# Kernel tuning notes

Hardware: AMD Instinct MI355X
Metric: run time of the kernel (lower is better)

The kernel has to match this reference:

```python
import jax, jax.numpy as jnp
import numpy as np

N = 50000      # n_nodes
E = 300000     # n_edges
R = 32         # n_relations
D = 256        # embedding_dim
H = 128        # bilstm_hidden_size (2H == D so gate dims line up, as the source requires)
I = 64         # input_dim (time-series feature dim)
B = 4096       # batch
S = 50         # seq_len
HOPS = 2       # context_hops


def setup_inputs() -> dict:
    key = jax.random.key(0)
    ks = jax.random.split(key, 20)
    sc = 0.02
    inp = {
        "ts": jax.random.normal(ks[0], (B, S, I), jnp.float32),
        "node_emb": jax.random.normal(ks[1], (N, D), jnp.float32) * sc,
        "rel_w": jax.random.normal(ks[2], (R, D), jnp.float32) * sc + 1.0,
        "gate_W": jax.random.normal(ks[3], (D, 2 * D), jnp.float32) * sc,
        "gate_b": jnp.zeros((D,), jnp.float32),
        "risk_W1": jax.random.normal(ks[4], (D, D), jnp.float32) * sc,
        "risk_b1": jnp.zeros((D,), jnp.float32),
        "risk_W2": jax.random.normal(ks[5], (D, D), jnp.float32) * sc,
        "risk_b2": jnp.zeros((D,), jnp.float32),
        # BiLSTM encoder params (torch gate order i,f,g,o), fwd + bwd directions
        "Wih_f": jax.random.normal(ks[6], (4 * H, I), jnp.float32) * sc,
        "Whh_f": jax.random.normal(ks[7], (4 * H, H), jnp.float32) * sc,
        "b_f": jnp.zeros((4 * H,), jnp.float32),
        "Wih_b": jax.random.normal(ks[8], (4 * H, I), jnp.float32) * sc,
        "Whh_b": jax.random.normal(ks[9], (4 * H, H), jnp.float32) * sc,
        "b_b": jnp.zeros((4 * H,), jnp.float32),
        "edge_index": jax.random.randint(ks[10], (2, E), 0, N, jnp.int32),
        "edge_type": jax.random.randint(ks[11], (E,), 0, R, jnp.int32),
        "node_indexes": jax.random.randint(ks[12], (B,), 0, N, jnp.int32),
    }
    return inp


def _lstm_dir(x, Wih, Whh, b, reverse):
    # x: [B, S, I] -> outputs [B, S, H]
    def step(carry, xt):
        h, c = carry
        g = xt @ Wih.T + h @ Whh.T + b          # [B, 4H]
        i, f, gg, o = jnp.split(g, 4, axis=-1)
        c = jax.nn.sigmoid(f) * c + jax.nn.sigmoid(i) * jnp.tanh(gg)
        h = jax.nn.sigmoid(o) * jnp.tanh(c)
        return (h, c), h
    h0 = jnp.zeros((x.shape[0], Whh.shape[1]), x.dtype)
    xs = jnp.swapaxes(x, 0, 1)                   # [S, B, I]
    _, hs = jax.lax.scan(step, (h0, h0), xs, reverse=reverse)
    return jnp.swapaxes(hs, 0, 1)                # [B, S, H]


def _gcn(emb, head, tail, edge_type, rel_w, n_hops):
    # relation-weighted multi-hop message passing: gather -> relation scale -> scatter-mean
    deg = jax.ops.segment_sum(jnp.ones((head.shape[0],), emb.dtype), head, num_segments=N)
    deg = jnp.clip(deg, 1.0)[:, None]
    out = emb
    acc = emb
    for _ in range(n_hops):
        msg = out[tail] * rel_w[edge_type]                      # [E, D]
        out = jax.ops.segment_sum(msg, head, num_segments=N) / deg
        acc = acc + out
    return acc / (n_hops + 1.0)


def reference(ts, node_emb, rel_w, gate_W, gate_b, risk_W1, risk_b1, risk_W2,
              risk_b2, Wih_f, Whh_f, b_f, Wih_b, Whh_b, b_b,
              edge_index, edge_type, node_indexes):
    head, tail = edge_index[0], edge_index[1]
    all_emb = _gcn(node_emb, head, tail, edge_type, rel_w, HOPS)
    struct = all_emb[node_indexes]                              # [B, D]
    # BiLSTM encoder, temporal embedding = mean over time of [B,S,2H]
    hf = _lstm_dir(ts, Wih_f, Whh_f, b_f, reverse=False)
    hb = _lstm_dir(ts, Wih_b, Whh_b, b_b, reverse=True)
    temporal = jnp.concatenate([hf, hb], axis=-1).mean(axis=1)  # [B, 2H] == [B, D]
    cat = jnp.concatenate([struct, temporal], axis=-1)          # [B, 2D]
    gate = jax.nn.sigmoid(cat @ gate_W.T + gate_b)              # [B, D]
    merged = gate * struct + (1.0 - gate) * temporal
    risk = jnp.tanh(merged @ risk_W1.T + risk_b1) @ risk_W2.T + risk_b2
    return jax.nn.sigmoid(risk.sum(axis=-1))                    # [B]
```

## Files before the change

### kernel.cpp

```cpp
#include <hip/hip_runtime.h>

#define N_NODES 50000
#define N_EDGES 300000
#define DIM 256
#define HID 128
#define INP 64
#define BATCH 4096
#define SEQ 50
#define SCAN_BLOCKS 196

typedef float f32x2 __attribute__((ext_vector_type(2)));
typedef float f32x4 __attribute__((ext_vector_type(4)));
typedef __bf16 bf16x2 __attribute__((ext_vector_type(2)));
typedef __bf16 bf16x4 __attribute__((ext_vector_type(4)));
typedef __bf16 bf16x8 __attribute__((ext_vector_type(8)));

#define L2E  1.4426950408889634f
#define L2E2 2.8853900817779268f

__device__ __forceinline__ float sigmoidf_(float x) {
    return __builtin_amdgcn_rcpf(1.0f + __expf(-x));
}
__device__ __forceinline__ float tanhf_(float x) {
    return 1.0f - 2.0f * __builtin_amdgcn_rcpf(1.0f + __expf(2.0f * x));
}
__device__ __forceinline__ float sigp_(float y) {
    return __builtin_amdgcn_rcpf(1.0f + __builtin_amdgcn_exp2f(-y));
}
__device__ __forceinline__ float tanhp_(float y) {
    return 1.0f - 2.0f * __builtin_amdgcn_rcpf(1.0f + __builtin_amdgcn_exp2f(y));
}
__device__ __forceinline__ float tanhc_(float x) {
    return 1.0f - 2.0f * __builtin_amdgcn_rcpf(1.0f + __builtin_amdgcn_exp2f(x * L2E2));
}

__device__ __forceinline__ void barrier_lds_only() {
    asm volatile("s_waitcnt lgkmcnt(0)" ::: "memory");
    __builtin_amdgcn_s_barrier();
}

__global__ void k_prep(const float* __restrict__ Wih_f, const float* __restrict__ Whh_f,
                       const float* __restrict__ Wih_b, const float* __restrict__ Whh_b,
                       const float* __restrict__ gate_W, const float* __restrict__ risk_W1,
                       const float* __restrict__ risk_W2, const float* __restrict__ risk_b2,
                       const float* __restrict__ node_emb,
                       __bf16* __restrict__ w2frag, __bf16* __restrict__ gwp,
                       __bf16* __restrict__ w1p, float* __restrict__ w2s,
                       int* __restrict__ deg, int* __restrict__ flagi,
                       __bf16* __restrict__ embh) {
    __shared__ float red[256];
    int bid = blockIdx.x, tid = threadIdx.x;
    if (bid < 768) {
        int idx = bid * 256 + tid;
        int dir = idx / 98304;
        int rem = idx % 98304;
        int frag = rem >> 9;
        int within = rem & 511;
        int lane = within >> 3, j = within & 7;
        int kc = frag % 6;
        int wg = frag / 6;
        int g = wg & 3, w = wg >> 2;
        int n = g * 128 + w * 16 + (lane & 15);
        int k = kc * 32 + (lane >> 4) * 8 + j;
        const float* Wih = dir ? Wih_b : Wih_f;
        const float* Whh = dir ? Whh_b : Whh_f;
        float v = (k < 64) ? Wih[n * 64 + k] : Whh[n * 128 + (k - 64)];
        float sc = (g == 2) ? L2E2 : L2E;
        w2frag[idx] = (__bf16)(v * sc);
    } else if (bid < 1280) {
        int idx = (bid - 768) * 256 + tid;
        int frag = idx >> 9, within = idx & 511;
        int lane = within >> 3, j = within & 7;
        int kc = frag % 16, T = frag / 16;
        int n = T * 16 + (lane & 15);
        int k = kc * 32 + (lane >> 4) * 8 + j;
        gwp[idx] = (__bf16)gate_W[(size_t)n * 512 + k];
    } else if (bid < 1536) {
        int idx = (bid - 1280) * 256 + tid;
        int frag = idx >> 9, within = idx & 511;
        int lane = within >> 3, j = within & 7;
        int kc = frag % 8, T = frag / 8;
        int n = T * 16 + (lane & 15);
        int k = kc * 32 + (lane >> 4) * 8 + j;
        w1p[idx] = (__bf16)risk_W1[(size_t)n * 256 + k];
    } else if (bid == 1536) {
        int k = tid;
        float s = 0.0f;
        for (int n = 0; n < 256; n++) s += risk_W2[(size_t)n * 256 + k];
        w2s[k] = s;
        red[k] = risk_b2[k];
        __syncthreads();
        for (int st = 128; st > 0; st >>= 1) {
            if (k < st) red[k] += red[k + st];
            __syncthreads();
        }
        if (k == 0) w2s[256] = red[0];
    } else if (bid < 1733) {
        int i = (bid - 1537) * 256 + tid;
        if (i < N_NODES) deg[i] = 0;
    } else if (bid < 1782) {
        int i = (bid - 1733) * 256 + tid;
        flagi[i] = 0;
    } else {
        int idx = (bid - 1782) * 2048 + tid * 8;
        f32x4 a = *(const f32x4*)(node_emb + idx);
        f32x4 b = *(const f32x4*)(node_emb + idx + 4);
        bf16x8 o;
        o[0] = (__bf16)a.x; o[1] = (__bf16)a.y; o[2] = (__bf16)a.z; o[3] = (__bf16)a.w;
        o[4] = (__bf16)b.x; o[5] = (__bf16)b.y; o[6] = (__bf16)b.z; o[7] = (__bf16)b.w;
        *(bf16x8*)(embh + idx) = o;
    }
}


__global__ void k_hist(const int* __restrict__ head, int* __restrict__ deg) {
    int e = blockIdx.x * 256 + threadIdx.x;
    if (e < N_EDGES) atomicAdd(&deg[head[e]], 1);
}

__global__ void k_bsum(const int* __restrict__ deg, int* __restrict__ bsum) {
    __shared__ int red[256];
    int n = blockIdx.x * 256 + threadIdx.x;
    red[threadIdx.x] = (n < N_NODES) ? deg[n] : 0;
    __syncthreads();
    for (int st = 128; st > 0; st >>= 1) {
        if (threadIdx.x < st) red[threadIdx.x] += red[threadIdx.x + st];
        __syncthreads();
    }
    if (threadIdx.x == 0) bsum[blockIdx.x] = red[0];
}

__global__ void k_scanb(const int* __restrict__ bsum, int* __restrict__ boff) {
    __shared__ int s[256];
    int i = threadIdx.x;
    int v = (i < SCAN_BLOCKS) ? bsum[i] : 0;
    s[i] = v;
    __syncthreads();
    for (int st = 1; st < 256; st <<= 1) {
        int add = (i >= st) ? s[i - st] : 0;
        __syncthreads();
        s[i] += add;
        __syncthreads();
    }
    boff[i] = s[i] - v;
}

__global__ void k_scan2(const int* __restrict__ deg, const int* __restrict__ boff,
                        int* __restrict__ offsets, int* __restrict__ cursor) {
    __shared__ int s[256];
    int i = threadIdx.x;
    int n = blockIdx.x * 256 + i;
    int v = (n < N_NODES) ? deg[n] : 0;
    s[i] = v;
    __syncthreads();
    for (int st = 1; st < 256; st <<= 1) {
        int add = (i >= st) ? s[i - st] : 0;
        __syncthreads();
        s[i] += add;
        __syncthreads();
    }
    if (n < N_NODES) {
        int off = boff[blockIdx.x] + s[i] - v;
        offsets[n] = off;
        cursor[n] = off;
    }
    if (n == 0) offsets[N_NODES] = N_EDGES;
}

__global__ void k_place(const int* __restrict__ head, const int* __restrict__ tail,
                        const int* __restrict__ etype, int* __restrict__ cursor,
                        int* __restrict__ sorted) {
    int e = blockIdx.x * 256 + threadIdx.x;
    if (e >= N_EDGES) return;
    int h = head[e];
    int pos = atomicAdd(&cursor[h], 1);
    sorted[pos] = tail[e] | (etype[e] << 16);
}

__global__ void k_flag(const int* __restrict__ nidx, const int* __restrict__ offsets,
                       const int* __restrict__ sorted, char* __restrict__ flag) {
    int tid = threadIdx.x;
    int w = tid >> 6, lane = tid & 63;
    int b = blockIdx.x * 4 + w;
    int n = nidx[b];
    if (lane == 0) flag[n] = 1;
    int s = offsets[n], e = offsets[n + 1];
    for (int j = s + lane; j < e; j += 64) flag[sorted[j] & 0xFFFF] = 1;
}

__global__ void k_gather(const int* __restrict__ offsets, const int* __restrict__ sorted,
                         const float* __restrict__ relw, const __bf16* __restrict__ srch,
                         const char* __restrict__ flag, __bf16* __restrict__ dst) {
    int tid = threadIdx.x;
    int w = tid >> 6, lane = tid & 63;
    int n = blockIdx.x * 4 + w;
    if (n >= N_NODES) return;
    if (!flag[n]) return;
    int s = offsets[n], e = offsets[n + 1];
    f32x4 acc0 = (f32x4){0.f, 0.f, 0.f, 0.f};
    f32x4 acc1 = (f32x4){0.f, 0.f, 0.f, 0.f};
    f32x4 acc2 = (f32x4){0.f, 0.f, 0.f, 0.f};
    f32x4 acc3 = (f32x4){0.f, 0.f, 0.f, 0.f};
    int j = s;
    for (; j + 4 <= e; j += 4) {
        int p0 = sorted[j], p1 = sorted[j + 1], p2 = sorted[j + 2], p3 = sorted[j + 3];
        bf16x4 v0 = *(const bf16x4*)(srch + (size_t)(p0 & 0xFFFF) * DIM + lane * 4);
        bf16x4 v1 = *(const bf16x4*)(srch + (size_t)(p1 & 0xFFFF) * DIM + lane * 4);
        bf16x4 v2 = *(const bf16x4*)(srch + (size_t)(p2 & 0xFFFF) * DIM + lane * 4);
        bf16x4 v3 = *(const bf16x4*)(srch + (size_t)(p3 & 0xFFFF) * DIM + lane * 4);
        f32x4 f0 = (f32x4){(float)v0[0], (float)v0[1], (float)v0[2], (float)v0[3]};
        f32x4 f1 = (f32x4){(float)v1[0], (float)v1[1], (float)v1[2], (float)v1[3]};
        f32x4 f2 = (f32x4){(float)v2[0], (float)v2[1], (float)v2[2], (float)v2[3]};
        f32x4 f3 = (f32x4){(float)v3[0], (float)v3[1], (float)v3[2], (float)v3[3]};
        acc0 += f0 * *(const f32x4*)(relw + (p0 >> 16) * DIM + lane * 4);
        acc1 += f1 * *(const f32x4*)(relw + (p1 >> 16) * DIM + lane * 4);
        acc2 += f2 * *(const f32x4*)(relw + (p2 >> 16) * DIM + lane * 4);
        acc3 += f3 * *(const f32x4*)(relw + (p3 >> 16) * DIM + lane * 4);
    }
    for (; j < e; j++) {
        int p0 = sorted[j];
        bf16x4 v0 = *(const bf16x4*)(srch + (size_t)(p0 & 0xFFFF) * DIM + lane * 4);
        f32x4 f0 = (f32x4){(float)v0[0], (float)v0[1], (float)v0[2], (float)v0[3]};
        acc0 += f0 * *(const f32x4*)(relw + (p0 >> 16) * DIM + lane * 4);
    }
    acc0 = (acc0 + acc1) + (acc2 + acc3);
    float inv = 1.0f / fmaxf((float)(e - s), 1.0f);
    acc0 *= inv;
    bf16x4 o;
    o[0] = (__bf16)acc0.x; o[1] = (__bf16)acc0.y; o[2] = (__bf16)acc0.z; o[3] = (__bf16)acc0.w;
    *(bf16x4*)(dst + (size_t)n * DIM + lane * 4) = o;
}

__global__ void k_gather2(const int* __restrict__ nidx, const int* __restrict__ offsets,
                          const int* __restrict__ sorted, const float* __restrict__ relw,
                          const __bf16* __restrict__ out1h, const __bf16* __restrict__ embh,
                          float* __restrict__ structb) {
    int tid = threadIdx.x;
    int w = tid >> 6, lane = tid & 63;
    int b = blockIdx.x * 4 + w;
    int n = nidx[b];
    int s = offsets[n], e = offsets[n + 1];
    f32x4 acc0 = (f32x4){0.f, 0.f, 0.f, 0.f};
    f32x4 acc1 = (f32x4){0.f, 0.f, 0.f, 0.f};
    f32x4 acc2 = (f32x4){0.f, 0.f, 0.f, 0.f};
    f32x4 acc3 = (f32x4){0.f, 0.f, 0.f, 0.f};
    int j = s;
    for (; j + 4 <= e; j += 4) {
        int p0 = sorted[j], p1 = sorted[j + 1], p2 = sorted[j + 2], p3 = sorted[j + 3];
        bf16x4 v0 = *(const bf16x4*)(out1h + (size_t)(p0 & 0xFFFF) * DIM + lane * 4);
        bf16x4 v1 = *(const bf16x4*)(out1h + (size_t)(p1 & 0xFFFF) * DIM + lane * 4);
        bf16x4 v2 = *(const bf16x4*)(out1h + (size_t)(p2 & 0xFFFF) * DIM + lane * 4);
        bf16x4 v3 = *(const bf16x4*)(out1h + (size_t)(p3 & 0xFFFF) * DIM + lane * 4);
        f32x4 f0 = (f32x4){(float)v0[0], (float)v0[1], (float)v0[2], (float)v0[3]};
        f32x4 f1 = (f32x4){(float)v1[0], (float)v1[1], (float)v1[2], (float)v1[3]};
        f32x4 f2 = (f32x4){(float)v2[0], (float)v2[1], (float)v2[2], (float)v2[3]};
        f32x4 f3 = (f32x4){(float)v3[0], (float)v3[1], (float)v3[2], (float)v3[3]};
        acc0 += f0 * *(const f32x4*)(relw + (p0 >> 16) * DIM + lane * 4);
        acc1 += f1 * *(const f32x4*)(relw + (p1 >> 16) * DIM + lane * 4);
        acc2 += f2 * *(const f32x4*)(relw + (p2 >> 16) * DIM + lane * 4);
        acc3 += f3 * *(const f32x4*)(relw + (p3 >> 16) * DIM + lane * 4);
    }
    for (; j < e; j++) {
        int p0 = sorted[j];
        bf16x4 v0 = *(const bf16x4*)(out1h + (size_t)(p0 & 0xFFFF) * DIM + lane * 4);
        f32x4 f0 = (f32x4){(float)v0[0], (float)v0[1], (float)v0[2], (float)v0[3]};
        acc0 += f0 * *(const f32x4*)(relw + (p0 >> 16) * DIM + lane * 4);
    }
    acc0 = (acc0 + acc1) + (acc2 + acc3);
    float inv = 1.0f / fmaxf((float)(e - s), 1.0f);
    f32x4 o2 = acc0 * inv;
    bf16x4 eh = *(const bf16x4*)(embh + (size_t)n * DIM + lane * 4);
    bf16x4 o1h = *(const bf16x4*)(out1h + (size_t)n * DIM + lane * 4);
    f32x4 e0 = (f32x4){(float)eh[0], (float)eh[1], (float)eh[2], (float)eh[3]};
    f32x4 o1 = (f32x4){(float)o1h[0], (float)o1h[1], (float)o1h[2], (float)o1h[3]};
    *(f32x4*)(structb + (size_t)b * DIM + lane * 4) = (e0 + o1 + o2) * (1.0f / 3.0f);
}

__launch_bounds__(512)
__global__ void k_lstm(const float* __restrict__ ts, const __bf16* __restrict__ w2frag,
                       const float* __restrict__ b_f, const float* __restrict__ b_b,
                       float* __restrict__ temporal) {
    int dir = blockIdx.y;
    int btile = blockIdx.x;
    int tid = threadIdx.x;
    int w = tid >> 6;
    int lane = tid & 63;
    int col = lane & 15, quad = lane >> 4;

    __shared__ __align__(16) __bf16 SA[2 * 16 * 200];
    __shared__ __align__(16) __bf16 SB[2 * 16 * 200];

    for (int i = tid; i < 2048; i += 512) {
        int m = i >> 7, k = i & 127;
        SA[m * 200 + 64 + k] = (__bf16)0.0f;
        SB[m * 200 + 64 + k] = (__bf16)0.0f;
    }

    const float* bias = dir ? b_b : b_f;
    f32x4 bva[4];
#pragma unroll
    for (int g = 0; g < 4; g++) {
        float b = bias[g * 128 + w * 16 + col] * ((g == 2) ? L2E2 : L2E);
        bva[g] = (f32x4){b, b, b, b};
    }

    const __bf16* wbase = w2frag + (size_t)dir * 98304 + (size_t)w * 12288;
    bf16x8 wreg[24];
#pragma unroll
    for (int f = 0; f < 24; f++) {
        wreg[f] = *(const bf16x8*)(wbase + (f << 9) + lane * 8);
    }

    int sm = tid >> 5, sc = (tid & 31) * 2;
    const float* xbA = ts + ((size_t)(btile * 32 + sm) * SEQ) * INP + sc;
    const float* xbB = ts + ((size_t)(btile * 32 + 16 + sm) * SEQ) * INP + sc;
    int t0i = dir ? (SEQ - 1) : 0;
    int t1i = dir ? (SEQ - 2) : 1;
    {
        f32x2 xa = *(const f32x2*)(xbA + (size_t)t0i * INP);
        f32x2 xb = *(const f32x2*)(xbB + (size_t)t0i * INP);
        bf16x2 va; va[0] = (__bf16)xa.x; va[1] = (__bf16)xa.y;
        bf16x2 vb; vb[0] = (__bf16)xb.x; vb[1] = (__bf16)xb.y;
        *(bf16x2*)&SA[sm * 200 + sc] = va;
        *(bf16x2*)&SB[sm * 200 + sc] = vb;
    }
    f32x2 xpreA = *(const f32x2*)(xbA + (size_t)t1i * INP);
    f32x2 xpreB = *(const f32x2*)(xbB + (size_t)t1i * INP);
    int xdelta = dir ? -INP : INP;
    const float* pA = xbA + (size_t)(dir ? (SEQ - 3) : 2) * INP;
    const float* pB = xbB + (size_t)(dir ? (SEQ - 3) : 2) * INP;

    f32x4 cA = (f32x4){0.f, 0.f, 0.f, 0.f}, hsA = cA;
    f32x4 cB = cA, hsB = cA;
    f32x4 accA[4], accB[4];
    int hwr = quad * 4 * 200 + 64 + w * 16 + col;
    int ard = col * 200 + quad * 8;
    barrier_lds_only();

    {
        bf16x8 a0 = *(const bf16x8*)&SA[ard];
#pragma unroll
        for (int g = 0; g < 4; g++)
            accA[g] = __builtin_amdgcn_mfma_f32_16x16x32_bf16(a0, wreg[g * 6], bva[g], 0, 0, 0);
    }
#pragma unroll
    for (int kc = 1; kc < 6; kc++) {
        bf16x8 a0 = *(const bf16x8*)&SA[ard + kc * 32];
#pragma unroll
        for (int g = 0; g < 4; g++)
            accA[g] = __builtin_amdgcn_mfma_f32_16x16x32_bf16(a0, wreg[g * 6 + kc], accA[g], 0, 0, 0);
    }

    for (int t = 0; t < SEQ; t++) {
        int cb = (t & 1) * 3200;
        int nb = ((t + 1) & 1) * 3200;

        f32x2 xnA;
        bool ld = (t + 2 < SEQ);
        if (ld) { xnA = *(const f32x2*)pA; pA += xdelta; }
        {
            bf16x8 a0 = *(const bf16x8*)&SB[cb + ard];
#pragma unroll
            for (int g = 0; g < 4; g++)
                accB[g] = __builtin_amdgcn_mfma_f32_16x16x32_bf16(a0, wreg[g * 6], bva[g], 0, 0, 0);
        }
#pragma unroll
        for (int kc = 1; kc < 6; kc++) {
            bf16x8 a0 = *(const bf16x8*)&SB[cb + ard + kc * 32];
#pragma unroll
            for (int g = 0; g < 4; g++)
                accB[g] = __builtin_amdgcn_mfma_f32_16x16x32_bf16(a0, wreg[g * 6 + kc], accB[g], 0, 0, 0);
        }
#pragma unroll
        for (int r = 0; r < 4; r++) {
            float c = sigp_(accA[1][r]) * cA[r] + sigp_(accA[0][r]) * tanhp_(accA[2][r]);
            float h = sigp_(accA[3][r]) * tanhc_(c);
            cA[r] = c;
            hsA[r] += h;
            SA[nb + hwr + r * 200] = (__bf16)h;
        }
        if (t + 1 < SEQ) {
            bf16x2 v; v[0] = (__bf16)xpreA.x; v[1] = (__bf16)xpreA.y;
            *(bf16x2*)&SA[nb + sm * 200 + sc] = v;
            if (ld) xpreA = xnA;
        }
        barrier_lds_only();

        f32x2 xnB;
        if (ld) { xnB = *(const f32x2*)pB; pB += xdelta; }
        if (t + 1 < SEQ) {
            {
                bf16x8 a0 = *(const bf16x8*)&SA[nb + ard];
#pragma unroll
                for (int g = 0; g < 4; g++)
                    accA[g] = __builtin_amdgcn_mfma_f32_16x16x32_bf16(a0, wreg[g * 6], bva[g], 0, 0, 0);
            }
#pragma unroll
            for (int kc = 1; kc < 6; kc++) {
                bf16x8 a0 = *(const bf16x8*)&SA[nb + ard + kc * 32];
#pragma unroll
                for (int g = 0; g < 4; g++)
                    accA[g] = __builtin_amdgcn_mfma_f32_16x16x32_bf16(a0, wreg[g * 6 + kc], accA[g], 0, 0, 0);
            }
        }
#pragma unroll
        for (int r = 0; r < 4; r++) {
            float c = sigp_(accB[1][r]) * cB[r] + sigp_(accB[0][r]) * tanhp_(accB[2][r]);
            float h = sigp_(accB[3][r]) * tanhc_(c);
            cB[r] = c;
            hsB[r] += h;
            SB[nb + hwr + r * 200] = (__bf16)h;
        }
        if (t + 1 < SEQ) {
            bf16x2 v; v[0] = (__bf16)xpreB.x; v[1] = (__bf16)xpreB.y;
            *(bf16x2*)&SB[nb + sm * 200 + sc] = v;
            if (ld) xpreB = xnB;
        }
        barrier_lds_only();
    }

#pragma unroll
    for (int r = 0; r < 4; r++) {
        int j = w * 16 + col;
        int bA = btile * 32 + quad * 4 + r;
        int bB = bA + 16;
        temporal[(size_t)bA * 256 + dir * 128 + j] = hsA[r] * (1.0f / SEQ);
        temporal[(size_t)bB * 256 + dir * 128 + j] = hsB[r] * (1.0f / SEQ);
    }
}


__launch_bounds__(256)
__global__ void k_head(const float* __restrict__ structb, const float* __restrict__ temporal,
                       const __bf16* __restrict__ gwp, const __bf16* __restrict__ w1p,
                       const float* __restrict__ gate_b, const float* __restrict__ risk_b1,
                       const float* __restrict__ w2s, float* __restrict__ out) {
    int bt = blockIdx.x;
    int tid = threadIdx.x;
    int w = tid >> 6, lane = tid & 63;
    int col = lane & 15, quad = lane >> 4;

    __shared__ __align__(16) __bf16 cat[16][520];
    __shared__ __align__(16) __bf16 mbuf[16][264];
    __shared__ float sacc[16];

    for (int i = tid; i < 16 * 512; i += 256) {
        int m = i >> 9, k = i & 511;
        int b = bt * 16 + m;
        float v = (k < 256) ? structb[(size_t)b * 256 + k]
                            : temporal[(size_t)b * 256 + (k - 256)];
        cat[m][k] = (__bf16)v;
    }
    if (tid < 16) sacc[tid] = 0.0f;
    __syncthreads();

    f32x4 acc[4];
#pragma unroll
    for (int ct = 0; ct < 4; ct++) {
        float b = gate_b[w * 64 + ct * 16 + col];
        acc[ct] = (f32x4){b, b, b, b};
    }
#pragma unroll
    for (int kc = 0; kc < 16; kc++) {
        bf16x8 a = *(const bf16x8*)&cat[col][kc * 32 + quad * 8];
#pragma unroll
        for (int ct = 0; ct < 4; ct++) {
            bf16x8 bf = *(const bf16x8*)(gwp + (((w * 4 + ct) * 16 + kc) << 9) + lane * 8);
            acc[ct] = __builtin_amdgcn_mfma_f32_16x16x32_bf16(a, bf, acc[ct], 0, 0, 0);
        }
    }
#pragma unroll
    for (int ct = 0; ct < 4; ct++) {
        int n = w * 64 + ct * 16 + col;
#pragma unroll
        for (int r = 0; r < 4; r++) {
            int m = quad * 4 + r;
            int b = bt * 16 + m;
            float g = sigmoidf_(acc[ct][r]);
            float s = structb[(size_t)b * 256 + n];
            float tm = temporal[(size_t)b * 256 + n];
            mbuf[m][n] = (__bf16)(g * s + (1.0f - g) * tm);
        }
    }
    __syncthreads();

    f32x4 acc2[4];
#pragma unroll
    for (int ct = 0; ct < 4; ct++) {
        float b = risk_b1[w * 64 + ct * 16 + col];
        acc2[ct] = (f32x4){b, b, b, b};
    }
#pragma unroll
    for (int kc = 0; kc < 8; kc++) {
        bf16x8 a = *(const bf16x8*)&mbuf[col][kc * 32 + quad * 8];
#pragma unroll
        for (int ct = 0; ct < 4; ct++) {
            bf16x8 bf = *(const bf16x8*)(w1p + (((w * 4 + ct) * 8 + kc) << 9) + lane * 8);
            acc2[ct] = __builtin_amdgcn_mfma_f32_16x16x32_bf16(a, bf, acc2[ct], 0, 0, 0);
        }
    }
    float part[4] = {0.f, 0.f, 0.f, 0.f};
#pragma unroll
    for (int ct = 0; ct < 4; ct++) {
        int n = w * 64 + ct * 16 + col;
        float wv = w2s[n];
#pragma unroll
        for (int r = 0; r < 4; r++) {
            part[r] += tanhf_(acc2[ct][r]) * wv;
        }
    }
#pragma unroll
    for (int off = 1; off < 16; off <<= 1) {
#pragma unroll
        for (int r = 0; r < 4; r++) part[r] += __shfl_xor(part[r], off, 64);
    }
    if (col == 0) {
#pragma unroll
        for (int r = 0; r < 4; r++) atomicAdd(&sacc[quad * 4 + r], part[r]);
    }
    __syncthreads();
    if (tid < 16) out[bt * 16 + tid] = sigmoidf_(sacc[tid] + w2s[256]);
}


extern "C" void kernel_launch(void* const* d_in, const int* in_sizes, int n_in,
                              void* d_out, int out_size, void* d_ws, size_t ws_size,
                              hipStream_t stream) {
    const float* ts       = (const float*)d_in[0];
    const float* node_emb = (const float*)d_in[1];
    const float* rel_w    = (const float*)d_in[2];
    const float* gate_W   = (const float*)d_in[3];
    const float* gate_b   = (const float*)d_in[4];
    const float* risk_W1  = (const float*)d_in[5];
    const float* risk_b1  = (const float*)d_in[6];
    const float* risk_W2  = (const float*)d_in[7];
    const float* risk_b2  = (const float*)d_in[8];
    const float* Wih_f    = (const float*)d_in[9];
    const float* Whh_f    = (const float*)d_in[10];
    const float* b_f      = (const float*)d_in[11];
    const float* Wih_b    = (const float*)d_in[12];
    const float* Whh_b    = (const float*)d_in[13];
    const float* b_b      = (const float*)d_in[14];
    const int* edge_index = (const int*)d_in[15];
    const int* edge_type  = (const int*)d_in[16];
    const int* node_idx   = (const int*)d_in[17];
    const int* head = edge_index;
    const int* tail = edge_index + N_EDGES;
    float* out = (float*)d_out;

    char* ws = (char*)d_ws;
    const size_t o_deg      = 0;
    const size_t o_flagbuf  = 200704;
    const size_t o_bsum     = o_flagbuf + 50176;
    const size_t o_boff     = o_bsum + 1024;
    const size_t o_offsets  = o_boff + 1024;
    const size_t o_cursor   = o_offsets + 200960;
    const size_t o_sorted   = o_cursor + 200704;
    const size_t o_out1     = o_sorted + 1200128;
    const size_t o_embh     = o_out1 + 25600000;
    const size_t o_temporal = o_embh + 25600000;
    const size_t o_struct   = o_temporal + 4194304;
    const size_t o_gwp      = o_struct + 4194304;
    const size_t o_w1p      = o_gwp + 262144;
    const size_t o_w2s      = o_w1p + 131072;
    const size_t o_w2frag   = o_w2s + 2048;

    int*    deg      = (int*)(ws + o_deg);
    char*   flag     = (char*)(ws + o_flagbuf);
    int*    flagi    = (int*)(ws + o_flagbuf);
    int*    bsum     = (int*)(ws + o_bsum);
    int*    boff     = (int*)(ws + o_boff);
    int*    offsets  = (int*)(ws + o_offsets);
    int*    cursor   = (int*)(ws + o_cursor);
    int*    sorted   = (int*)(ws + o_sorted);
    __bf16* out1h    = (__bf16*)(ws + o_out1);
    __bf16* embh     = (__bf16*)(ws + o_embh);
    float*  temporal = (float*)(ws + o_temporal);
    float*  structb  = (float*)(ws + o_struct);
    __bf16* gwp      = (__bf16*)(ws + o_gwp);
    __bf16* w1p      = (__bf16*)(ws + o_w1p);
    float*  w2s      = (float*)(ws + o_w2s);
    __bf16* w2frag   = (__bf16*)(ws + o_w2frag);

    k_prep<<<8032, 256, 0, stream>>>(Wih_f, Whh_f, Wih_b, Whh_b, gate_W, risk_W1,
                                     risk_W2, risk_b2, node_emb, w2frag, gwp, w1p,
                                     w2s, deg, flagi, embh);
    k_hist<<<(N_EDGES + 255) / 256, 256, 0, stream>>>(head, deg);
    k_bsum<<<SCAN_BLOCKS, 256, 0, stream>>>(deg, bsum);
    k_scanb<<<1, 256, 0, stream>>>(bsum, boff);
    k_scan2<<<SCAN_BLOCKS, 256, 0, stream>>>(deg, boff, offsets, cursor);
    k_place<<<(N_EDGES + 255) / 256, 256, 0, stream>>>(head, tail, edge_type, cursor, sorted);
    k_flag<<<BATCH / 4, 256, 0, stream>>>(node_idx, offsets, sorted, flag);
    k_gather<<<(N_NODES + 3) / 4, 256, 0, stream>>>(offsets, sorted, rel_w, embh, flag, out1h);
    k_lstm<<<dim3(BATCH / 32, 2), 512, 0, stream>>>(ts, w2frag, b_f, b_b, temporal);
    k_gather2<<<BATCH / 4, 256, 0, stream>>>(node_idx, offsets, sorted, rel_w, out1h, embh, structb);
    k_head<<<BATCH / 16, 256, 0, stream>>>(structb, temporal, gwp, w1p, gate_b, risk_b1, w2s, out);
}
```

Measured before the change: 317.0 us.

## Split LSTM kernel into one 16-row tile per block, doubling grid

The LSTM kernel no longer interleaves two 16-row batch tiles (A/B ping-pong) within a block. Each block now handles a single 16-row tile, and the grid doubles from 128x2 to 256x2 blocks. This exposes more blocks to fill the GPU's compute units and halves LDS use per block. In exchange it gives up the intra-block overlap in which one tile's MFMA work hid the other tile's activation math and barrier latency, and every block must reload the recurrent weights into registers.

```diff
diff --git a/kernel.cpp b/kernel.cpp
--- a/kernel.cpp
+++ b/kernel.cpp
@@ -231,6 +231,104 @@
     *(bf16x4*)(dst + (size_t)n * DIM + lane * 4) = o;
 }
 
+__launch_bounds__(512)
+__global__ void k_lstm(const float* __restrict__ ts, const __bf16* __restrict__ w2frag,
+                       const float* __restrict__ b_f, const float* __restrict__ b_b,
+                       float* __restrict__ temporal) {
+    int dir = blockIdx.y;
+    int btile = blockIdx.x;
+    int tid = threadIdx.x;
+    int w = tid >> 6;
+    int lane = tid & 63;
+    int col = lane & 15, quad = lane >> 4;
+
+    __shared__ __align__(16) __bf16 S[2 * 16 * 200];
+
+    for (int i = tid; i < 2048; i += 512) {
+        int m = i >> 7, k = i & 127;
+        S[m * 200 + 64 + k] = (__bf16)0.0f;
+    }
+
+    const float* bias = dir ? b_b : b_f;
+    f32x4 bva[4];
+#pragma unroll
+    for (int g = 0; g < 4; g++) {
+        float b = bias[g * 128 + w * 16 + col] * ((g == 2) ? L2E2 : L2E);
+        bva[g] = (f32x4){b, b, b, b};
+    }
+
+    const __bf16* wbase = w2frag + (size_t)dir * 98304 + (size_t)w * 12288;
+    bf16x8 wreg[24];
+#pragma unroll
+    for (int f = 0; f < 24; f++) {
+        wreg[f] = *(const bf16x8*)(wbase + (f << 9) + lane * 8);
+    }
+
+    int sm = tid >> 5, sc = (tid & 31) * 2;
+    const float* xb = ts + ((size_t)(btile * 16 + sm) * SEQ) * INP + sc;
+    int t0i = dir ? (SEQ - 1) : 0;
+    int t1i = dir ? (SEQ - 2) : 1;
+    {
+        f32x2 xa = *(const f32x2*)(xb + (size_t)t0i * INP);
+        bf16x2 va; va[0] = (__bf16)xa.x; va[1] = (__bf16)xa.y;
+        *(bf16x2*)&S[sm * 200 + sc] = va;
+    }
+    f32x2 xpre = *(const f32x2*)(xb + (size_t)t1i * INP);
+    int xdelta = dir ? -INP : INP;
+    const float* p = xb + (size_t)(dir ? (SEQ - 3) : 2) * INP;
+
+    f32x4 c = (f32x4){0.f, 0.f, 0.f, 0.f}, hs = c;
+    f32x4 acc[4];
+    int hwr = quad * 4 * 200 + 64 + w * 16 + col;
+    int ard = col * 200 + quad * 8;
+    barrier_lds_only();
+
+    for (int t = 0; t < SEQ; t++) {
+        int cb = (t & 1) * 3200;
+        int nb = ((t + 1) & 1) * 3200;
+
+        f32x2 xn;
+        bool ld = (t + 2 < SEQ);
+        if (ld) { xn = *(const f32x2*)p; p += xdelta; }
+
+        {
+            bf16x8 a0 = *(const bf16x8*)&S[cb + ard];
+#pragma unroll
+            for (int g = 0; g < 4; g++)
+                acc[g] = __builtin_amdgcn_mfma_f32_16x16x32_bf16(a0, wreg[g * 6], bva[g], 0, 0, 0);
+        }
+#pragma unroll
+        for (int kc = 1; kc < 6; kc++) {
+            bf16x8 a0 = *(const bf16x8*)&S[cb + ard + kc * 32];
+#pragma unroll
+            for (int g = 0; g < 4; g++)
+                acc[g] = __builtin_amdgcn_mfma_f32_16x16x32_bf16(a0, wreg[g * 6 + kc], acc[g], 0, 0, 0);
+        }
+
+#pragma unroll
+        for (int r = 0; r < 4; r++) {
+            float cc = sigp_(acc[1][r]) * c[r] + sigp_(acc[0][r]) * tanhp_(acc[2][r]);
+            float h = sigp_(acc[3][r]) * tanhc_(cc);
+            c[r] = cc;
+            hs[r] += h;
+            S[nb + hwr + r * 200] = (__bf16)h;
+        }
+        if (t + 1 < SEQ) {
+            bf16x2 v; v[0] = (__bf16)xpre.x; v[1] = (__bf16)xpre.y;
+            *(bf16x2*)&S[nb + sm * 200 + sc] = v;
+            if (ld) xpre = xn;
+        }
+        barrier_lds_only();
+    }
+
+#pragma unroll
+    for (int r = 0; r < 4; r++) {
+        int j = w * 16 + col;
+        int b = btile * 16 + quad * 4 + r;
+        temporal[(size_t)b * 256 + dir * 128 + j] = hs[r] * (1.0f / SEQ);
+    }
+}
+
 __global__ void k_gather2(const int* __restrict__ nidx, const int* __restrict__ offsets,
                           const int* __restrict__ sorted, const float* __restrict__ relw,
                           const __bf16* __restrict__ out1h, const __bf16* __restrict__ embh,
@@ -276,159 +374,6 @@
     *(f32x4*)(structb + (size_t)b * DIM + lane * 4) = (e0 + o1 + o2) * (1.0f / 3.0f);
 }
 
-__launch_bounds__(512)
-__global__ void k_lstm(const float* __restrict__ ts, const __bf16* __restrict__ w2frag,
-                       const float* __restrict__ b_f, const float* __restrict__ b_b,
-                       float* __restrict__ temporal) {
-    int dir = blockIdx.y;
-    int btile = blockIdx.x;
-    int tid = threadIdx.x;
-    int w = tid >> 6;
-    int lane = tid & 63;
-    int col = lane & 15, quad = lane >> 4;
-
-    __shared__ __align__(16) __bf16 SA[2 * 16 * 200];
-    __shared__ __align__(16) __bf16 SB[2 * 16 * 200];
-
-    for (int i = tid; i < 2048; i += 512) {
-        int m = i >> 7, k = i & 127;
-        SA[m * 200 + 64 + k] = (__bf16)0.0f;
-        SB[m * 200 + 64 + k] = (__bf16)0.0f;
-    }
-
-    const float* bias = dir ? b_b : b_f;
-    f32x4 bva[4];
-#pragma unroll
-    for (int g = 0; g < 4; g++) {
-        float b = bias[g * 128 + w * 16 + col] * ((g == 2) ? L2E2 : L2E);
-        bva[g] = (f32x4){b, b, b, b};
-    }
-
-    const __bf16* wbase = w2frag + (size_t)dir * 98304 + (size_t)w * 12288;
-    bf16x8 wreg[24];
-#pragma unroll
-    for (int f = 0; f < 24; f++) {
-        wreg[f] = *(const bf16x8*)(wbase + (f << 9) + lane * 8);
-    }
-
-    int sm = tid >> 5, sc = (tid & 31) * 2;
-    const float* xbA = ts + ((size_t)(btile * 32 + sm) * SEQ) * INP + sc;
-    const float* xbB = ts + ((size_t)(btile * 32 + 16 + sm) * SEQ) * INP + sc;
-    int t0i = dir ? (SEQ - 1) : 0;
-    int t1i = dir ? (SEQ - 2) : 1;
-    {
-        f32x2 xa = *(const f32x2*)(xbA + (size_t)t0i * INP);
-        f32x2 xb = *(const f32x2*)(xbB + (size_t)t0i * INP);
-        bf16x2 va; va[0] = (__bf16)xa.x; va[1] = (__bf16)xa.y;
-        bf16x2 vb; vb[0] = (__bf16)xb.x; vb[1] = (__bf16)xb.y;
-        *(bf16x2*)&SA[sm * 200 + sc] = va;
-        *(bf16x2*)&SB[sm * 200 + sc] = vb;
-    }
-    f32x2 xpreA = *(const f32x2*)(xbA + (size_t)t1i * INP);
-    f32x2 xpreB = *(const f32x2*)(xbB + (size_t)t1i * INP);
-    int xdelta = dir ? -INP : INP;
-    const float* pA = xbA + (size_t)(dir ? (SEQ - 3) : 2) * INP;
-    const float* pB = xbB + (size_t)(dir ? (SEQ - 3) : 2) * INP;
-
-    f32x4 cA = (f32x4){0.f, 0.f, 0.f, 0.f}, hsA = cA;
-    f32x4 cB = cA, hsB = cA;
-    f32x4 accA[4], accB[4];
-    int hwr = quad * 4 * 200 + 64 + w * 16 + col;
-    int ard = col * 200 + quad * 8;
-    barrier_lds_only();
-
-    {
-        bf16x8 a0 = *(const bf16x8*)&SA[ard];
-#pragma unroll
-        for (int g = 0; g < 4; g++)
-            accA[g] = __builtin_amdgcn_mfma_f32_16x16x32_bf16(a0, wreg[g * 6], bva[g], 0, 0, 0);
-    }
-#pragma unroll
-    for (int kc = 1; kc < 6; kc++) {
-        bf16x8 a0 = *(const bf16x8*)&SA[ard + kc * 32];
-#pragma unroll
-        for (int g = 0; g < 4; g++)
-            accA[g] = __builtin_amdgcn_mfma_f32_16x16x32_bf16(a0, wreg[g * 6 + kc], accA[g], 0, 0, 0);
-    }
-
-    for (int t = 0; t < SEQ; t++) {
-        int cb = (t & 1) * 3200;
-        int nb = ((t + 1) & 1) * 3200;
-
-        f32x2 xnA;
-        bool ld = (t + 2 < SEQ);
-        if (ld) { xnA = *(const f32x2*)pA; pA += xdelta; }
-        {
-            bf16x8 a0 = *(const bf16x8*)&SB[cb + ard];
-#pragma unroll
-            for (int g = 0; g < 4; g++)
-                accB[g] = __builtin_amdgcn_mfma_f32_16x16x32_bf16(a0, wreg[g * 6], bva[g], 0, 0, 0);
-        }
-#pragma unroll
-        for (int kc = 1; kc < 6; kc++) {
-            bf16x8 a0 = *(const bf16x8*)&SB[cb + ard + kc * 32];
-#pragma unroll
-            for (int g = 0; g < 4; g++)
-                accB[g] = __builtin_amdgcn_mfma_f32_16x16x32_bf16(a0, wreg[g * 6 + kc], accB[g], 0, 0, 0);
-        }
-#pragma unroll
-        for (int r = 0; r < 4; r++) {
-            float c = sigp_(accA[1][r]) * cA[r] + sigp_(accA[0][r]) * tanhp_(accA[2][r]);
-            float h = sigp_(accA[3][r]) * tanhc_(c);
-            cA[r] = c;
-            hsA[r] += h;
-            SA[nb + hwr + r * 200] = (__bf16)h;
-        }
-        if (t + 1 < SEQ) {
-            bf16x2 v; v[0] = (__bf16)xpreA.x; v[1] = (__bf16)xpreA.y;
-            *(bf16x2*)&SA[nb + sm * 200 + sc] = v;
-            if (ld) xpreA = xnA;
-        }
-        barrier_lds_only();
-
-        f32x2 xnB;
-        if (ld) { xnB = *(const f32x2*)pB; pB += xdelta; }
-        if (t + 1 < SEQ) {
-            {
-                bf16x8 a0 = *(const bf16x8*)&SA[nb + ard];
-#pragma unroll
-                for (int g = 0; g < 4; g++)
-                    accA[g] = __builtin_amdgcn_mfma_f32_16x16x32_bf16(a0, wreg[g * 6], bva[g], 0, 0, 0);
-            }
-#pragma unroll
-            for (int kc = 1; kc < 6; kc++) {
-                bf16x8 a0 = *(const bf16x8*)&SA[nb + ard + kc * 32];
-#pragma unroll
-                for (int g = 0; g < 4; g++)
-                    accA[g] = __builtin_amdgcn_mfma_f32_16x16x32_bf16(a0, wreg[g * 6 + kc], accA[g], 0, 0, 0);
-            }
-        }
-#pragma unroll
-        for (int r = 0; r < 4; r++) {
-            float c = sigp_(accB[1][r]) * cB[r] + sigp_(accB[0][r]) * tanhp_(accB[2][r]);
-            float h = sigp_(accB[3][r]) * tanhc_(c);
-            cB[r] = c;
-            hsB[r] += h;
-            SB[nb + hwr + r * 200] = (__bf16)h;
-        }
-        if (t + 1 < SEQ) {
-            bf16x2 v; v[0] = (__bf16)xpreB.x; v[1] = (__bf16)xpreB.y;
-            *(bf16x2*)&SB[nb + sm * 200 + sc] = v;
-            if (ld) xpreB = xnB;
-        }
-        barrier_lds_only();
-    }
-
-#pragma unroll
-    for (int r = 0; r < 4; r++) {
-        int j = w * 16 + col;
-        int bA = btile * 32 + quad * 4 + r;
-        int bB = bA + 16;
-        temporal[(size_t)bA * 256 + dir * 128 + j] = hsA[r] * (1.0f / SEQ);
-        temporal[(size_t)bB * 256 + dir * 128 + j] = hsB[r] * (1.0f / SEQ);
-    }
-}
-
 
 __launch_bounds__(256)
 __global__ void k_head(const float* __restrict__ structb, const float* __restrict__ temporal,
@@ -592,7 +537,7 @@
     k_place<<<(N_EDGES + 255) / 256, 256, 0, stream>>>(head, tail, edge_type, cursor, sorted);
     k_flag<<<BATCH / 4, 256, 0, stream>>>(node_idx, offsets, sorted, flag);
     k_gather<<<(N_NODES + 3) / 4, 256, 0, stream>>>(offsets, sorted, rel_w, embh, flag, out1h);
-    k_lstm<<<dim3(BATCH / 32, 2), 512, 0, stream>>>(ts, w2frag, b_f, b_b, temporal);
+    k_lstm<<<dim3(BATCH / 16, 2), 512, 0, stream>>>(ts, w2frag, b_f, b_b, temporal);
     k_gather2<<<BATCH / 4, 256, 0, stream>>>(node_idx, offsets, sorted, rel_w, out1h, embh, structb);
     k_head<<<BATCH / 16, 256, 0, stream>>>(structb, temporal, gwp, w1p, gate_b, risk_b1, w2s, out);
 }
```

New measurement: 329.3 us. +3.9%, slower.
